# Performance work log

Measured on AMD Instinct MI355X. Metric: run time of the kernel, lower is better.

## Reference

```python
import jax, jax.numpy as jnp
import numpy as np

B, LQ, LK, D, H = 4, 1024, 1024, 512, 8
HD = D // H
NEG_SLOPE = 0.2


def setup_inputs() -> dict:
    key = jax.random.key(0)
    k1, k2, k3, k4, k5 = jax.random.split(key, 5)
    query = jax.random.normal(k1, (B, LQ, D), dtype=jnp.float32)
    key_t = jax.random.normal(k2, (B, LK, D), dtype=jnp.float32)
    value = jax.random.normal(k3, (B, LK, D), dtype=jnp.float32)
    mask = jnp.ones((B, LQ, LK), dtype=jnp.int32)
    # xavier-uniform-like init for params
    limW = float(np.sqrt(6.0 / (D + D)))
    W = jax.random.uniform(k4, (D, D), minval=-limW, maxval=limW, dtype=jnp.float32)
    lima = float(np.sqrt(6.0 / (H + 2 * HD)))
    a = jax.random.uniform(k5, (1, H, 2 * HD), minval=-lima, maxval=lima, dtype=jnp.float32)
    return {"query": query, "key": key_t, "value": value, "mask": mask, "W": W, "a": a}


def reference(query, key, value, mask, W, a):
    b, lq, d = query.shape
    lk = key.shape[1]
    h = a.shape[1]
    hd = a.shape[2] // 2
    # shared linear projection (nn.Linear: x @ W.T)
    Q = (query @ W.T).reshape(b, lq, h, hd)
    K = (key @ W.T).reshape(b, lk, h, hd)
    V = (value @ W.T).reshape(b, lk, h, hd)
    # a^T [Q || K] = a_q . Q + a_k . K  (avoids the (b,lq,lk,h,2hd) concat)
    a_q = a[0, :, :hd]  # (h, hd)
    a_k = a[0, :, hd:]
    sq = jnp.einsum('bqhd,hd->bhq', Q, a_q)
    sk = jnp.einsum('bkhd,hd->bhk', K, a_k)
    scores = sq[:, :, :, None] + sk[:, :, None, :]  # (b, h, lq, lk)
    scores = jnp.where(scores >= 0, scores, NEG_SLOPE * scores)  # LeakyReLU
    scores = jnp.where(mask[:, None, :, :] == 0, -jnp.inf, scores)
    attn = jax.nn.softmax(scores, axis=-1)
    attn = jnp.where(jnp.isnan(attn), 0.0, attn)  # fully-masked rows -> 0
    out = jnp.einsum('bhqk,bkhd->bqhd', attn, V).reshape(b, lq, d)
    return out
```

## Files before the change

### kernel.cpp

```cpp
#include <hip/hip_runtime.h>
#include <hip/hip_bf16.h>

#define NEG_SLOPE 0.2f

constexpr int B = 4, LQ = 1024, LK = 1024, D = 512, H = 8, HD = 64;

typedef __attribute__((ext_vector_type(8))) short bf16x8;
typedef __attribute__((ext_vector_type(4))) float f32x4;

static __device__ __forceinline__ ushort f2bf(float x) {
  return __builtin_bit_cast(ushort, __float2bfloat16(x));
}
static __device__ __forceinline__ float bf2f(ushort u) {
  return __bfloat162float(__builtin_bit_cast(__hip_bfloat16, u));
}

__global__ void prep_wqwk(const float* __restrict__ W, const float* __restrict__ a,
                          float* __restrict__ wq, float* __restrict__ wk) {
  int tid = blockIdx.x * blockDim.x + threadIdx.x;
  int h = tid >> 9, j = tid & 511;
  const float* aq = a + h * 2 * HD;
  const float* ak = aq + HD;
  float accq = 0.f, acck = 0.f;
#pragma unroll 8
  for (int d = 0; d < HD; ++d) {
    float w = W[(size_t)(h * HD + d) * D + j];
    accq = fmaf(aq[d], w, accq);
    acck = fmaf(ak[d], w, acck);
  }
  wq[tid] = accq;
  wk[tid] = acck;
}

__global__ __launch_bounds__(256) void fused_aux(
    const float* __restrict__ query, const float* __restrict__ key,
    const float* __restrict__ value, const int* __restrict__ mask,
    const float* __restrict__ W,
    const float* __restrict__ wq, const float* __restrict__ wk,
    ushort* __restrict__ val_hi, ushort* __restrict__ val_lo,
    ushort* __restrict__ w_hi, ushort* __restrict__ w_lo,
    unsigned int* __restrict__ mbits,
    float* __restrict__ sq, float* __restrict__ sk) {
  int blk = blockIdx.x, tid = threadIdx.x;
  if (blk < 2304) {
    constexpr int VAL4 = B * LK * D / 4;
    int idx = blk * 256 + tid;
    const float* src;
    ushort *dhi, *dlo;
    int off;
    if (idx < VAL4) { src = value; dhi = val_hi; dlo = val_lo; off = idx; }
    else           { src = W;     dhi = w_hi;   dlo = w_lo;   off = idx - VAL4; }
    float4 x = ((const float4*)src)[off];
    float xs[4] = {x.x, x.y, x.z, x.w};
    ushort hs[4], ls[4];
#pragma unroll
    for (int i = 0; i < 4; ++i) {
      hs[i] = f2bf(xs[i]);
      ls[i] = f2bf(xs[i] - bf2f(hs[i]));
    }
    ((ushort4*)dhi)[off] = make_ushort4(hs[0], hs[1], hs[2], hs[3]);
    ((ushort4*)dlo)[off] = make_ushort4(ls[0], ls[1], ls[2], ls[3]);
  } else if (blk < 4352) {
    int gw = ((blk - 2304) * 256 + tid) >> 6;
    int lane = tid & 63;
#pragma unroll
    for (int it = 0; it < 8; ++it) {
      int wv = gw * 8 + it;
      int mv = mask[(size_t)wv * 64 + lane];
      unsigned long long bal = __ballot(mv != 0);
      if (lane == 0) *(unsigned long long*)&mbits[wv * 2] = bal;
    }
  } else {
    int gw = ((blk - 4352) * 256 + tid) >> 6;
    int lane = tid & 63;
    bool isK = gw >= B * LQ;
    int row = isK ? gw - B * LQ : gw;
    const float* x = (isK ? key : query) + (size_t)row * D + lane * 8;
    const float* wbase = isK ? wk : wq;
    float4 x0 = *(const float4*)x;
    float4 x1 = *(const float4*)(x + 4);
    float acc[H];
#pragma unroll
    for (int h = 0; h < H; ++h) {
      const float* w = wbase + h * D + lane * 8;
      float4 w0 = *(const float4*)w;
      float4 w1 = *(const float4*)(w + 4);
      acc[h] = x0.x * w0.x + x0.y * w0.y + x0.z * w0.z + x0.w * w0.w +
               x1.x * w1.x + x1.y * w1.y + x1.z * w1.z + x1.w * w1.w;
    }
#pragma unroll
    for (int off = 32; off > 0; off >>= 1) {
#pragma unroll
      for (int h = 0; h < H; ++h) acc[h] += __shfl_xor(acc[h], off, 64);
    }
    if (lane == 0) {
      int b = row >> 10, pos = row & 1023;
      float* dst = isK ? sk : sq;
#pragma unroll
      for (int h = 0; h < H; ++h) dst[((size_t)(b * H + h) << 10) + pos] = acc[h];
    }
  }
}

__global__ __launch_bounds__(256) void vproj_mfma(
    const ushort* __restrict__ val_hi, const ushort* __restrict__ val_lo,
    const ushort* __restrict__ w_hi, const ushort* __restrict__ w_lo,
    ushort* __restrict__ vt_hi, ushort* __restrict__ vt_lo) {
  __shared__ float vred[3][64][36];
  int c0 = blockIdx.x * 32, r0 = blockIdx.y * 64;
  int tid = threadIdx.x, w = tid >> 6, lane = tid & 63;
  int ln15 = lane & 15, kg = lane >> 4;
  f32x4 acc[4][2] = {};
  for (int step = 0; step < 4; ++step) {
    int kq = w * 128 + step * 32 + kg * 8;
    bf16x8 ah[4], al[4], bh[2], bl[2];
#pragma unroll
    for (int fm = 0; fm < 4; ++fm) {
      size_t off = (size_t)(r0 + fm * 16 + ln15) * D + kq;
      ah[fm] = *(const bf16x8*)&val_hi[off];
      al[fm] = *(const bf16x8*)&val_lo[off];
    }
#pragma unroll
    for (int fn = 0; fn < 2; ++fn) {
      size_t off = (size_t)(c0 + fn * 16 + ln15) * D + kq;
      bh[fn] = *(const bf16x8*)&w_hi[off];
      bl[fn] = *(const bf16x8*)&w_lo[off];
    }
#pragma unroll
    for (int fm = 0; fm < 4; ++fm)
#pragma unroll
      for (int fn = 0; fn < 2; ++fn) {
        acc[fm][fn] = __builtin_amdgcn_mfma_f32_16x16x32_bf16(ah[fm], bh[fn], acc[fm][fn], 0, 0, 0);
        acc[fm][fn] = __builtin_amdgcn_mfma_f32_16x16x32_bf16(al[fm], bh[fn], acc[fm][fn], 0, 0, 0);
        acc[fm][fn] = __builtin_amdgcn_mfma_f32_16x16x32_bf16(ah[fm], bl[fn], acc[fm][fn], 0, 0, 0);
      }
  }
  if (w > 0) {
#pragma unroll
    for (int fm = 0; fm < 4; ++fm)
#pragma unroll
      for (int fn = 0; fn < 2; ++fn)
        *(f32x4*)&vred[w - 1][lane][(fm * 2 + fn) * 4] = acc[fm][fn];
  }
  __syncthreads();
  if (w == 0) {
#pragma unroll
    for (int fm = 0; fm < 4; ++fm)
#pragma unroll
      for (int fn = 0; fn < 2; ++fn) {
#pragma unroll
        for (int k = 0; k < 3; ++k)
          acc[fm][fn] += *(const f32x4*)&vred[k][lane][(fm * 2 + fn) * 4];
        int rrow = r0 + fm * 16 + (lane >> 4) * 4;
        int col = c0 + fn * 16 + ln15;
        int bb = rrow >> 10, kk = rrow & 1023;
        int hh = col >> 6, dd = col & 63;
        size_t base = ((size_t)((bb * H + hh) * HD + dd) << 10) + kk;
        ushort hv[4], lv[4];
#pragma unroll
        for (int r = 0; r < 4; ++r) {
          float v = acc[fm][fn][r];
          hv[r] = f2bf(v);
          lv[r] = f2bf(v - bf2f(hv[r]));
        }
        *(ushort4*)&vt_hi[base] = make_ushort4(hv[0], hv[1], hv[2], hv[3]);
        *(ushort4*)&vt_lo[base] = make_ushort4(lv[0], lv[1], lv[2], lv[3]);
      }
  }
}

__global__ __launch_bounds__(256) void attn_mfma(
    const float* __restrict__ sq, const float* __restrict__ sk,
    const unsigned int* __restrict__ mbits,
    const ushort* __restrict__ vt_hi, const ushort* __restrict__ vt_lo,
    float* __restrict__ out) {
  __shared__ float sks[LK];
  __shared__ float ared[2][64][36];
  __shared__ float lred[2][16];
  __shared__ float linv_s[2][16];
  int bid = blockIdx.x;
  int xcd = bid & 7, slot = bid >> 3;
  int bh = xcd * 4 + (slot & 3), qt = slot >> 2;
  int b = bh >> 3, h = bh & 7;
  int q0 = qt * 32;
  int tid = threadIdx.x, w = tid >> 6, lane = tid & 63;
  int strip = w & 1, khalf = w >> 1;
  int ln15 = lane & 15, kg = lane >> 4;
  int qs = q0 + strip * 16 + ln15;
#pragma unroll
  for (int i = 0; i < 4; ++i) sks[i * 256 + tid] = sk[((size_t)bh << 10) + i * 256 + tid];
  float sqv = sq[((size_t)bh << 10) + qs];
  const unsigned int* mrow = mbits + ((size_t)(b << 10) + qs) * (LK / 32);
  const ushort* vhbase = vt_hi + (((size_t)bh * HD) << 10);
  const ushort* vlbase = vt_lo + (((size_t)bh * HD) << 10);
  __syncthreads();
  f32x4 acc[4] = {};
  float lsum = 0.f;
  for (int tile = 0; tile < 4; ++tile) {
    int kt0 = khalf * 512 + tile * 128;
#pragma unroll
    for (int ks = 0; ks < 4; ++ks) {
      int kb = kt0 + ks * 32;
      unsigned int wb = mrow[kb >> 5];
      bf16x8 bhv[4], blv[4];
#pragma unroll
      for (int df = 0; df < 4; ++df) {
        size_t off = ((size_t)(df * 16 + ln15) << 10) + kb + kg * 8;
        bhv[df] = *(const bf16x8*)&vhbase[off];
        blv[df] = *(const bf16x8*)&vlbase[off];
      }
      float skv[8];
      *(float4*)&skv[0] = *(const float4*)&sks[kb + kg * 8];
      *(float4*)&skv[4] = *(const float4*)&sks[kb + kg * 8 + 4];
      bf16x8 phi, plo;
#pragma unroll
      for (int i = 0; i < 8; ++i) {
        float s = sqv + skv[i];
        float f = fmaxf(s, NEG_SLOPE * s);
        float p = ((wb >> (kg * 8 + i)) & 1u) ? __expf(f - 8.0f) : 0.f;
        lsum += p;
        ushort hb = f2bf(p);
        phi[i] = (short)hb;
        plo[i] = (short)f2bf(p - bf2f(hb));
      }
#pragma unroll
      for (int df = 0; df < 4; ++df) {
        acc[df] = __builtin_amdgcn_mfma_f32_16x16x32_bf16(phi, bhv[df], acc[df], 0, 0, 0);
        acc[df] = __builtin_amdgcn_mfma_f32_16x16x32_bf16(plo, bhv[df], acc[df], 0, 0, 0);
        acc[df] = __builtin_amdgcn_mfma_f32_16x16x32_bf16(phi, blv[df], acc[df], 0, 0, 0);
      }
    }
  }
  lsum += __shfl_xor(lsum, 16, 64);
  lsum += __shfl_xor(lsum, 32, 64);
  if (khalf == 1) {
#pragma unroll
    for (int df = 0; df < 4; ++df)
      *(f32x4*)&ared[strip][lane][df * 4] = acc[df];
    if (lane < 16) lred[strip][lane] = lsum;
  }
  __syncthreads();
  if (khalf == 0) {
#pragma unroll
    for (int df = 0; df < 4; ++df)
      acc[df] += *(const f32x4*)&ared[strip][lane][df * 4];
    lsum += lred[strip][ln15];
    if (lane < 16) linv_s[strip][lane] = (lsum > 0.f) ? 1.f / lsum : 0.f;
#pragma unroll
    for (int df = 0; df < 4; ++df) {
#pragma unroll
      for (int r = 0; r < 4; ++r) {
        int crow = (lane >> 4) * 4 + r;
        int qrow = q0 + strip * 16 + crow;
        float inv = linv_s[strip][crow];
        int col = h * HD + df * 16 + ln15;
        out[((size_t)(b << 10) + qrow) * D + col] = acc[df][r] * inv;
      }
    }
  }
}

extern "C" void kernel_launch(void* const* d_in, const int* in_sizes, int n_in,
                              void* d_out, int out_size, void* d_ws, size_t ws_size,
                              hipStream_t stream) {
  const float* query = (const float*)d_in[0];
  const float* key   = (const float*)d_in[1];
  const float* value = (const float*)d_in[2];
  const int*   mask  = (const int*)d_in[3];
  const float* W     = (const float*)d_in[4];
  const float* a     = (const float*)d_in[5];
  float* out = (float*)d_out;

  char* ws = (char*)d_ws;
  float* wq = (float*)ws;                    ws += 4096 * 4;
  float* wk = (float*)ws;                    ws += 4096 * 4;
  float* sq = (float*)ws;                    ws += 32768 * 4;
  float* sk = (float*)ws;                    ws += 32768 * 4;
  ushort* val_hi = (ushort*)ws;              ws += (size_t)B * LK * D * 2;
  ushort* val_lo = (ushort*)ws;              ws += (size_t)B * LK * D * 2;
  ushort* w_hi = (ushort*)ws;                ws += (size_t)D * D * 2;
  ushort* w_lo = (ushort*)ws;                ws += (size_t)D * D * 2;
  ushort* vt_hi = (ushort*)ws;               ws += (size_t)B * H * HD * LK * 2;
  ushort* vt_lo = (ushort*)ws;               ws += (size_t)B * H * HD * LK * 2;
  unsigned int* mbits = (unsigned int*)ws;   ws += (size_t)B * LQ * LK / 32 * 4;

  prep_wqwk<<<dim3(16), dim3(256), 0, stream>>>(W, a, wq, wk);
  fused_aux<<<dim3(6400), dim3(256), 0, stream>>>(
      query, key, value, mask, W, wq, wk,
      val_hi, val_lo, w_hi, w_lo, mbits, sq, sk);
  vproj_mfma<<<dim3(D / 32, B * LK / 64), dim3(256), 0, stream>>>(
      val_hi, val_lo, w_hi, w_lo, vt_hi, vt_lo);
  attn_mfma<<<dim3(32 * LQ / 32), dim3(256), 0, stream>>>(
      sq, sk, mbits, vt_hi, vt_lo, out);
}
```

Before: 184.9 us.

## Factor LeakyReLU exp into precomputed key exponentials and retile V projection

The attention kernel drops the per-element exponential. It precomputes exp(sk-4) and exp(0.2*sk-4) per key in shared memory and forms each weight as max(E_k, exp(-0.8*sq)*F_k), which is exact because exp is monotone and LeakyReLU is a max of two linear terms. It also drops the low-bf16 half of P, which removes one MFMA per fragment but loses some precision, and computes the row sum with an MFMA against a ones vector. The V projection is retiled to 64x64 output tiles staged through shared memory with a 2x2 wave layout, replacing the cross-wave split-K reduction.

Result: faster. 169.5 us (-8.3%).

```diff
diff --git a/kernel.cpp b/kernel.cpp
--- a/kernel.cpp
+++ b/kernel.cpp
@@ -106,67 +106,71 @@
     const ushort* __restrict__ val_hi, const ushort* __restrict__ val_lo,
     const ushort* __restrict__ w_hi, const ushort* __restrict__ w_lo,
     ushort* __restrict__ vt_hi, ushort* __restrict__ vt_lo) {
-  __shared__ float vred[3][64][36];
-  int c0 = blockIdx.x * 32, r0 = blockIdx.y * 64;
+  __shared__ ushort as_hi[64][72], as_lo[64][72], bs_hi[64][72], bs_lo[64][72];
+  int r0 = blockIdx.x * 64, c0 = blockIdx.y * 64;
   int tid = threadIdx.x, w = tid >> 6, lane = tid & 63;
+  int wr = w >> 1, wc = w & 1;
   int ln15 = lane & 15, kg = lane >> 4;
-  f32x4 acc[4][2] = {};
-  for (int step = 0; step < 4; ++step) {
-    int kq = w * 128 + step * 32 + kg * 8;
-    bf16x8 ah[4], al[4], bh[2], bl[2];
-#pragma unroll
-    for (int fm = 0; fm < 4; ++fm) {
-      size_t off = (size_t)(r0 + fm * 16 + ln15) * D + kq;
-      ah[fm] = *(const bf16x8*)&val_hi[off];
-      al[fm] = *(const bf16x8*)&val_lo[off];
-    }
+  f32x4 acc[2][2] = {};
+  int srow = tid >> 2, scol = (tid & 3) * 16;
+  const size_t arow = (size_t)(r0 + srow) * D;
+  const size_t brow = (size_t)(c0 + srow) * D;
+  for (int k0 = 0; k0 < D; k0 += 64) {
+    float4 ra0 = *(const float4*)&val_hi[arow + k0 + scol];
+    float4 ra1 = *(const float4*)&val_hi[arow + k0 + scol + 8];
+    float4 rb0 = *(const float4*)&val_lo[arow + k0 + scol];
+    float4 rb1 = *(const float4*)&val_lo[arow + k0 + scol + 8];
+    float4 rc0 = *(const float4*)&w_hi[brow + k0 + scol];
+    float4 rc1 = *(const float4*)&w_hi[brow + k0 + scol + 8];
+    float4 rd0 = *(const float4*)&w_lo[brow + k0 + scol];
+    float4 rd1 = *(const float4*)&w_lo[brow + k0 + scol + 8];
+    __syncthreads();
+    *(float4*)&as_hi[srow][scol] = ra0; *(float4*)&as_hi[srow][scol + 8] = ra1;
+    *(float4*)&as_lo[srow][scol] = rb0; *(float4*)&as_lo[srow][scol + 8] = rb1;
+    *(float4*)&bs_hi[srow][scol] = rc0; *(float4*)&bs_hi[srow][scol + 8] = rc1;
+    *(float4*)&bs_lo[srow][scol] = rd0; *(float4*)&bs_lo[srow][scol + 8] = rd1;
+    __syncthreads();
+#pragma unroll
+    for (int ks2 = 0; ks2 < 2; ++ks2) {
+      bf16x8 ah[2], al[2], bh[2], bl[2];
+#pragma unroll
+      for (int f = 0; f < 2; ++f) {
+        int ra = wr * 32 + f * 16 + ln15;
+        ah[f] = *(const bf16x8*)&as_hi[ra][ks2 * 32 + kg * 8];
+        al[f] = *(const bf16x8*)&as_lo[ra][ks2 * 32 + kg * 8];
+        int rb = wc * 32 + f * 16 + ln15;
+        bh[f] = *(const bf16x8*)&bs_hi[rb][ks2 * 32 + kg * 8];
+        bl[f] = *(const bf16x8*)&bs_lo[rb][ks2 * 32 + kg * 8];
+      }
+#pragma unroll
+      for (int fm = 0; fm < 2; ++fm)
+#pragma unroll
+        for (int fn = 0; fn < 2; ++fn) {
+          acc[fm][fn] = __builtin_amdgcn_mfma_f32_16x16x32_bf16(ah[fm], bh[fn], acc[fm][fn], 0, 0, 0);
+          acc[fm][fn] = __builtin_amdgcn_mfma_f32_16x16x32_bf16(al[fm], bh[fn], acc[fm][fn], 0, 0, 0);
+          acc[fm][fn] = __builtin_amdgcn_mfma_f32_16x16x32_bf16(ah[fm], bl[fn], acc[fm][fn], 0, 0, 0);
+        }
+    }
+  }
+#pragma unroll
+  for (int fm = 0; fm < 2; ++fm)
 #pragma unroll
     for (int fn = 0; fn < 2; ++fn) {
-      size_t off = (size_t)(c0 + fn * 16 + ln15) * D + kq;
-      bh[fn] = *(const bf16x8*)&w_hi[off];
-      bl[fn] = *(const bf16x8*)&w_lo[off];
-    }
-#pragma unroll
-    for (int fm = 0; fm < 4; ++fm)
-#pragma unroll
-      for (int fn = 0; fn < 2; ++fn) {
-        acc[fm][fn] = __builtin_amdgcn_mfma_f32_16x16x32_bf16(ah[fm], bh[fn], acc[fm][fn], 0, 0, 0);
-        acc[fm][fn] = __builtin_amdgcn_mfma_f32_16x16x32_bf16(al[fm], bh[fn], acc[fm][fn], 0, 0, 0);
-        acc[fm][fn] = __builtin_amdgcn_mfma_f32_16x16x32_bf16(ah[fm], bl[fn], acc[fm][fn], 0, 0, 0);
+      int rrow = r0 + wr * 32 + fm * 16 + (lane >> 4) * 4;
+      int col = c0 + wc * 32 + fn * 16 + ln15;
+      int bb = rrow >> 10, kk = rrow & 1023;
+      int hh = col >> 6, dd = col & 63;
+      size_t base = ((size_t)((bb * H + hh) * HD + dd) << 10) + kk;
+      ushort hv[4], lv[4];
+#pragma unroll
+      for (int r = 0; r < 4; ++r) {
+        float v = acc[fm][fn][r];
+        hv[r] = f2bf(v);
+        lv[r] = f2bf(v - bf2f(hv[r]));
       }
-  }
-  if (w > 0) {
-#pragma unroll
-    for (int fm = 0; fm < 4; ++fm)
-#pragma unroll
-      for (int fn = 0; fn < 2; ++fn)
-        *(f32x4*)&vred[w - 1][lane][(fm * 2 + fn) * 4] = acc[fm][fn];
-  }
-  __syncthreads();
-  if (w == 0) {
-#pragma unroll
-    for (int fm = 0; fm < 4; ++fm)
-#pragma unroll
-      for (int fn = 0; fn < 2; ++fn) {
-#pragma unroll
-        for (int k = 0; k < 3; ++k)
-          acc[fm][fn] += *(const f32x4*)&vred[k][lane][(fm * 2 + fn) * 4];
-        int rrow = r0 + fm * 16 + (lane >> 4) * 4;
-        int col = c0 + fn * 16 + ln15;
-        int bb = rrow >> 10, kk = rrow & 1023;
-        int hh = col >> 6, dd = col & 63;
-        size_t base = ((size_t)((bb * H + hh) * HD + dd) << 10) + kk;
-        ushort hv[4], lv[4];
-#pragma unroll
-        for (int r = 0; r < 4; ++r) {
-          float v = acc[fm][fn][r];
-          hv[r] = f2bf(v);
-          lv[r] = f2bf(v - bf2f(hv[r]));
-        }
-        *(ushort4*)&vt_hi[base] = make_ushort4(hv[0], hv[1], hv[2], hv[3]);
-        *(ushort4*)&vt_lo[base] = make_ushort4(lv[0], lv[1], lv[2], lv[3]);
-      }
-  }
+      *(ushort4*)&vt_hi[base] = make_ushort4(hv[0], hv[1], hv[2], hv[3]);
+      *(ushort4*)&vt_lo[base] = make_ushort4(lv[0], lv[1], lv[2], lv[3]);
+    }
 }
 
 __global__ __launch_bounds__(256) void attn_mfma(
@@ -174,10 +178,8 @@
     const unsigned int* __restrict__ mbits,
     const ushort* __restrict__ vt_hi, const ushort* __restrict__ vt_lo,
     float* __restrict__ out) {
-  __shared__ float sks[LK];
-  __shared__ float ared[2][64][36];
-  __shared__ float lred[2][16];
-  __shared__ float linv_s[2][16];
+  __shared__ float skE_s[LK], skF_s[LK];
+  __shared__ float ared[2][64][24];
   int bid = blockIdx.x;
   int xcd = bid & 7, slot = bid >> 3;
   int bh = xcd * 4 + (slot & 3), qt = slot >> 2;
@@ -188,73 +190,79 @@
   int ln15 = lane & 15, kg = lane >> 4;
   int qs = q0 + strip * 16 + ln15;
 #pragma unroll
-  for (int i = 0; i < 4; ++i) sks[i * 256 + tid] = sk[((size_t)bh << 10) + i * 256 + tid];
+  for (int i = 0; i < 4; ++i) {
+    int j = i * 256 + tid;
+    float skv = sk[((size_t)bh << 10) + j];
+    skE_s[j] = __expf(skv - 4.0f);
+    skF_s[j] = __expf(0.2f * skv - 4.0f);
+  }
   float sqv = sq[((size_t)bh << 10) + qs];
-  const unsigned int* mrow = mbits + ((size_t)(b << 10) + qs) * (LK / 32);
+  float rq = __expf(-0.8f * sqv);
+  const uint4* mrowp = (const uint4*)(mbits + ((size_t)(b << 10) + qs) * (LK / 32) + khalf * 16);
+  uint4 mw0 = mrowp[0], mw1 = mrowp[1], mw2 = mrowp[2], mw3 = mrowp[3];
   const ushort* vhbase = vt_hi + (((size_t)bh * HD) << 10);
   const ushort* vlbase = vt_lo + (((size_t)bh * HD) << 10);
+  bf16x8 ones;
+#pragma unroll
+  for (int i = 0; i < 8; ++i) ones[i] = (short)0x3F80;
   __syncthreads();
   f32x4 acc[4] = {};
-  float lsum = 0.f;
-  for (int tile = 0; tile < 4; ++tile) {
-    int kt0 = khalf * 512 + tile * 128;
-#pragma unroll
-    for (int ks = 0; ks < 4; ++ks) {
-      int kb = kt0 + ks * 32;
-      unsigned int wb = mrow[kb >> 5];
-      bf16x8 bhv[4], blv[4];
-#pragma unroll
-      for (int df = 0; df < 4; ++df) {
-        size_t off = ((size_t)(df * 16 + ln15) << 10) + kb + kg * 8;
-        bhv[df] = *(const bf16x8*)&vhbase[off];
-        blv[df] = *(const bf16x8*)&vlbase[off];
-      }
-      float skv[8];
-      *(float4*)&skv[0] = *(const float4*)&sks[kb + kg * 8];
-      *(float4*)&skv[4] = *(const float4*)&sks[kb + kg * 8 + 4];
-      bf16x8 phi, plo;
-#pragma unroll
-      for (int i = 0; i < 8; ++i) {
-        float s = sqv + skv[i];
-        float f = fmaxf(s, NEG_SLOPE * s);
-        float p = ((wb >> (kg * 8 + i)) & 1u) ? __expf(f - 8.0f) : 0.f;
-        lsum += p;
-        ushort hb = f2bf(p);
-        phi[i] = (short)hb;
-        plo[i] = (short)f2bf(p - bf2f(hb));
-      }
-#pragma unroll
-      for (int df = 0; df < 4; ++df) {
-        acc[df] = __builtin_amdgcn_mfma_f32_16x16x32_bf16(phi, bhv[df], acc[df], 0, 0, 0);
-        acc[df] = __builtin_amdgcn_mfma_f32_16x16x32_bf16(plo, bhv[df], acc[df], 0, 0, 0);
-        acc[df] = __builtin_amdgcn_mfma_f32_16x16x32_bf16(phi, blv[df], acc[df], 0, 0, 0);
-      }
-    }
-  }
-  lsum += __shfl_xor(lsum, 16, 64);
-  lsum += __shfl_xor(lsum, 32, 64);
+  f32x4 acc5 = {};
+  unsigned int mwords[16] = {mw0.x, mw0.y, mw0.z, mw0.w, mw1.x, mw1.y, mw1.z, mw1.w,
+                             mw2.x, mw2.y, mw2.z, mw2.w, mw3.x, mw3.y, mw3.z, mw3.w};
+#pragma unroll
+  for (int t = 0; t < 16; ++t) {
+    int kb = khalf * 512 + t * 32;
+    unsigned int wb = mwords[t];
+    bf16x8 bhv[4], blv[4];
+#pragma unroll
+    for (int df = 0; df < 4; ++df) {
+      size_t off = ((size_t)(df * 16 + ln15) << 10) + kb + kg * 8;
+      bhv[df] = *(const bf16x8*)&vhbase[off];
+      blv[df] = *(const bf16x8*)&vlbase[off];
+    }
+    float ev[8], fv[8];
+    *(float4*)&ev[0] = *(const float4*)&skE_s[kb + kg * 8];
+    *(float4*)&ev[4] = *(const float4*)&skE_s[kb + kg * 8 + 4];
+    *(float4*)&fv[0] = *(const float4*)&skF_s[kb + kg * 8];
+    *(float4*)&fv[4] = *(const float4*)&skF_s[kb + kg * 8 + 4];
+    bf16x8 phi;
+#pragma unroll
+    for (int i = 0; i < 8; ++i) {
+      float pf = fmaxf(ev[i], rq * fv[i]);
+      float p = ((wb >> (kg * 8 + i)) & 1u) ? pf : 0.f;
+      phi[i] = (short)f2bf(p);
+    }
+#pragma unroll
+    for (int df = 0; df < 4; ++df) {
+      acc[df] = __builtin_amdgcn_mfma_f32_16x16x32_bf16(phi, bhv[df], acc[df], 0, 0, 0);
+      acc[df] = __builtin_amdgcn_mfma_f32_16x16x32_bf16(phi, blv[df], acc[df], 0, 0, 0);
+    }
+    acc5 = __builtin_amdgcn_mfma_f32_16x16x32_bf16(phi, ones, acc5, 0, 0, 0);
+  }
   if (khalf == 1) {
 #pragma unroll
     for (int df = 0; df < 4; ++df)
       *(f32x4*)&ared[strip][lane][df * 4] = acc[df];
-    if (lane < 16) lred[strip][lane] = lsum;
+    *(f32x4*)&ared[strip][lane][16] = acc5;
   }
   __syncthreads();
   if (khalf == 0) {
 #pragma unroll
     for (int df = 0; df < 4; ++df)
       acc[df] += *(const f32x4*)&ared[strip][lane][df * 4];
-    lsum += lred[strip][ln15];
-    if (lane < 16) linv_s[strip][lane] = (lsum > 0.f) ? 1.f / lsum : 0.f;
+    acc5 += *(const f32x4*)&ared[strip][lane][16];
+    float inv[4];
+#pragma unroll
+    for (int r = 0; r < 4; ++r) inv[r] = (acc5[r] > 0.f) ? 1.f / acc5[r] : 0.f;
 #pragma unroll
     for (int df = 0; df < 4; ++df) {
 #pragma unroll
       for (int r = 0; r < 4; ++r) {
         int crow = (lane >> 4) * 4 + r;
         int qrow = q0 + strip * 16 + crow;
-        float inv = linv_s[strip][crow];
         int col = h * HD + df * 16 + ln15;
-        out[((size_t)(b << 10) + qrow) * D + col] = acc[df][r] * inv;
+        out[((size_t)(b << 10) + qrow) * D + col] = acc[df][r] * inv[r];
       }
     }
   }
@@ -288,7 +296,7 @@
   fused_aux<<<dim3(6400), dim3(256), 0, stream>>>(
       query, key, value, mask, W, wq, wk,
       val_hi, val_lo, w_hi, w_lo, mbits, sq, sk);
-  vproj_mfma<<<dim3(D / 32, B * LK / 64), dim3(256), 0, stream>>>(
+  vproj_mfma<<<dim3(B * LK / 64, D / 64), dim3(256), 0, stream>>>(
       val_hi, val_lo, w_hi, w_lo, vt_hi, vt_lo);
   attn_mfma<<<dim3(32 * LQ / 32), dim3(256), 0, stream>>>(
       sq, sk, mbits, vt_hi, vt_lo, out);
```
